# Kernel optimization log

Measured on AMD Instinct MI355X. Metric: run time of the kernel, lower is better.

Reference implementation:

```python
import jax, jax.numpy as jnp
import numpy as np

DIM = 1024
HEADS = 16
HEAD_DIM = DIM // HEADS
B, S = 4, 4096


def setup_inputs() -> dict:
    key = jax.random.key(0)
    ks = jax.random.split(key, 8)
    sc = 1.0 / np.sqrt(DIM)
    return {
        "x": jax.random.normal(ks[0], (B, S, DIM), dtype=jnp.float32),
        "Wq": jax.random.normal(ks[1], (DIM, DIM), dtype=jnp.float32) * sc,
        "Wk": jax.random.normal(ks[2], (DIM, DIM), dtype=jnp.float32) * sc,
        "Wv": jax.random.normal(ks[3], (DIM, DIM), dtype=jnp.float32) * sc,
        "Wp": jax.random.normal(ks[4], (DIM, DIM), dtype=jnp.float32) * sc,
        "bp": jnp.zeros((DIM,), dtype=jnp.float32),
        "conv_w": jax.random.normal(ks[5], (DIM, 3), dtype=jnp.float32) * (1.0 / np.sqrt(3.0)),
        "conv_b": jnp.zeros((DIM,), dtype=jnp.float32),
    }


def reference(x, Wq, Wk, Wv, Wp, bp, conv_w, conv_b):
    b, s, d = x.shape
    # projections -> [b, h, n, hd] (torch Linear: x @ W.T)
    def split_heads(t):
        return t.reshape(b, s, HEADS, HEAD_DIM).transpose(0, 2, 1, 3)
    q = split_heads(x @ Wq.T)
    k = split_heads(x @ Wk.T)
    v = split_heads(x @ Wv.T)
    # ELU(+1) feature map
    q = jax.nn.elu(q) + 1.0
    k = jax.nn.elu(k) + 1.0
    # global kv-state and k-state
    kv_state = jnp.einsum('bhnd,bhne->bhde', k, v)   # [b,h,hd,hd]
    k_state = k.sum(axis=2)                          # [b,h,hd]
    attn_out = jnp.einsum('bhnd,bhde->bhne', q, kv_state)
    denom = jnp.maximum(jnp.einsum('bhnd,bhd->bhn', q, k_state), 1e-6)[..., None]
    attn_out = (attn_out / denom).transpose(0, 2, 1, 3).reshape(b, s, d)
    # depthwise conv1d, kernel=3, padding=1 (per-channel)
    xp = jnp.pad(x, ((0, 0), (1, 1), (0, 0)))        # [b, s+2, d]
    local = (xp[:, :-2, :] * conv_w[:, 0]
             + xp[:, 1:-1, :] * conv_w[:, 1]
             + xp[:, 2:, :] * conv_w[:, 2]) + conv_b
    return (attn_out + local) @ Wp.T + bp
```

## Files before the change

### kernel.cpp

```cpp
#include <hip/hip_runtime.h>
#include <hip/hip_bf16.h>
#include <stdint.h>

#define DIMN 1024
#define HEADS 16
#define HD 64
#define BATCH 4
#define SEQ 4096
#define M_TOT (BATCH*SEQ)

typedef __attribute__((ext_vector_type(8))) __bf16 bf16x8;
typedef __attribute__((ext_vector_type(4))) __bf16 bf16x4;
typedef __attribute__((ext_vector_type(4))) float f32x4;

__device__ __forceinline__ void gload_lds16(const void* g, void* l) {
  __builtin_amdgcn_global_load_lds(
      (const __attribute__((address_space(1))) void*)(uintptr_t)g,
      (__attribute__((address_space(3))) void*)(uint32_t)(uintptr_t)l,
      16, 0, 0);
}

__device__ __forceinline__ uint32_t swz128(uint32_t off) {
  return off ^ (((off >> 7) & 7) << 4);
}

__device__ __forceinline__ void lfence() { asm volatile("" ::: "memory"); }
__device__ __forceinline__ void barx() { lfence(); __builtin_amdgcn_s_barrier(); lfence(); }

__global__ __launch_bounds__(256) void cast_all_kernel(const float* __restrict__ x,
                                                       const float* __restrict__ wq,
                                                       const float* __restrict__ wk,
                                                       const float* __restrict__ wv,
                                                       const float* __restrict__ wp,
                                                       __bf16* __restrict__ xb,
                                                       __bf16* __restrict__ wqb,
                                                       __bf16* __restrict__ wkb,
                                                       __bf16* __restrict__ wvb,
                                                       __bf16* __restrict__ wpb) {
  int i = blockIdx.x * 256 + threadIdx.x;
  const float* src; __bf16* dst; int j;
  if (i < 4194304)      { src = x;  dst = xb;  j = i; }
  else {
    int t = i - 4194304;
    int w = t >> 18; j = t & 262143;
    if      (w == 0) { src = wq; dst = wqb; }
    else if (w == 1) { src = wk; dst = wkb; }
    else if (w == 2) { src = wv; dst = wvb; }
    else             { src = wp; dst = wpb; }
  }
  f32x4 v = ((const f32x4*)src)[j];
  bf16x4 o;
  o[0] = (__bf16)v[0]; o[1] = (__bf16)v[1]; o[2] = (__bf16)v[2]; o[3] = (__bf16)v[3];
  ((bf16x4*)dst)[j] = o;
}

template <int MODE, int NT>
__global__ __launch_bounds__(512, 2) void gemm256(const __bf16* __restrict__ A,
                                                  const __bf16* __restrict__ Bw,
                                                  void* __restrict__ Cout,
                                                  const float* __restrict__ bias) {
  __shared__ char lds[131072];
  const int KB = DIMN * 2;
  const int NKT = DIMN / 64;
  const int bid = blockIdx.x;
  const int x = bid & 7, jj = bid >> 3;
  const int n_t = jj % NT, m_t = (jj / NT) * 8 + x;
  const int m0 = m_t * 256, n0 = n_t * 256;
  const int tid = threadIdx.x;
  const int lane = tid & 63;
  const int wave = tid >> 6;
  const int wm = wave >> 2;
  const int wn = wave & 3;
  const int r16 = lane & 15, r4 = lane >> 4;

  const uint32_t s_off0 = tid * 16;
  const uint32_t s_off1 = 8192 + tid * 16;
  const uint32_t s_row0 = s_off0 >> 7, s_row1 = s_off1 >> 7;
  const uint32_t s_col0 = (s_off0 ^ ((s_row0 & 7) << 4)) & 127;
  const uint32_t s_col1 = (s_off1 ^ ((s_row1 & 7) << 4)) & 127;

  const char* Ab = (const char*)A + (size_t)m0 * KB;
  const char* Bb = (const char*)Bw + (size_t)n0 * KB;

  auto STAGE = [&](int op, int h, int kt, int b) {
    const char* gb = (op ? Bb : Ab) + (size_t)(h * 128) * KB + kt * 128;
    char* lb = lds + op * 65536 + b * 32768 + h * 16384;
    gload_lds16(gb + s_row0 * KB + s_col0, lb + s_off0);
    gload_lds16(gb + s_row1 * KB + s_col1, lb + s_off1);
  };

  uint32_t axk[2];
#pragma unroll
  for (int k = 0; k < 2; ++k) axk[k] = (uint32_t)(k * 64 + r4 * 16) ^ ((r16 & 7) << 4);

  f32x4 acc[8][4] = {};
  bf16x8 bc[4][2];

  STAGE(1, 0, 0, 0); STAGE(1, 1, 0, 0); STAGE(0, 0, 0, 0); STAGE(0, 1, 0, 0);
  STAGE(1, 0, 1, 1); STAGE(1, 1, 1, 1); STAGE(0, 0, 1, 1);
  asm volatile("s_waitcnt vmcnt(6)" ::: "memory");
  barx();

  for (int kt = 0; kt < NKT; ++kt) {
    const int p = kt & 1;
    const char* abuf = lds + p * 32768;
    const char* bbuf = lds + 65536 + p * 32768;

    {
      bf16x8 af[2][2];
#pragma unroll
      for (int nf = 0; nf < 4; ++nf)
#pragma unroll
        for (int k = 0; k < 2; ++k)
          bc[nf][k] = *(const bf16x8*)(bbuf + (nf >> 1) * 16384 +
                        (((nf & 1) * 64 + wn * 16 + r16) << 7) + axk[k]);
#pragma unroll
      for (int i = 0; i < 2; ++i)
#pragma unroll
        for (int k = 0; k < 2; ++k)
          af[i][k] = *(const bf16x8*)(abuf + ((i * 32 + wm * 16 + r16) << 7) + axk[k]);
      if (kt + 1 < NKT) STAGE(0, 1, kt + 1, (kt + 1) & 1);
      barx();
      __builtin_amdgcn_s_setprio(1);
#pragma unroll
      for (int i = 0; i < 2; ++i)
#pragma unroll
        for (int nf = 0; nf < 4; ++nf)
#pragma unroll
          for (int k = 0; k < 2; ++k)
            acc[i][nf] = __builtin_amdgcn_mfma_f32_16x16x32_bf16(bc[nf][k], af[i][k], acc[i][nf], 0, 0, 0);
      __builtin_amdgcn_s_setprio(0);
    }
    {
      bf16x8 af[2][2];
#pragma unroll
      for (int i = 0; i < 2; ++i)
#pragma unroll
        for (int k = 0; k < 2; ++k)
          af[i][k] = *(const bf16x8*)(abuf + (((2 + i) * 32 + wm * 16 + r16) << 7) + axk[k]);
      if (kt + 2 < NKT) STAGE(1, 0, kt + 2, p);
      barx();
      __builtin_amdgcn_s_setprio(1);
#pragma unroll
      for (int i = 0; i < 2; ++i)
#pragma unroll
        for (int nf = 0; nf < 4; ++nf)
#pragma unroll
          for (int k = 0; k < 2; ++k)
            acc[2 + i][nf] = __builtin_amdgcn_mfma_f32_16x16x32_bf16(bc[nf][k], af[i][k], acc[2 + i][nf], 0, 0, 0);
      __builtin_amdgcn_s_setprio(0);
    }
    {
      bf16x8 af[2][2];
#pragma unroll
      for (int i = 0; i < 2; ++i)
#pragma unroll
        for (int k = 0; k < 2; ++k)
          af[i][k] = *(const bf16x8*)(abuf + 16384 + ((i * 32 + wm * 16 + r16) << 7) + axk[k]);
      if (kt + 2 < NKT) STAGE(1, 1, kt + 2, p);
      barx();
      __builtin_amdgcn_s_setprio(1);
#pragma unroll
      for (int i = 0; i < 2; ++i)
#pragma unroll
        for (int nf = 0; nf < 4; ++nf)
#pragma unroll
          for (int k = 0; k < 2; ++k)
            acc[4 + i][nf] = __builtin_amdgcn_mfma_f32_16x16x32_bf16(bc[nf][k], af[i][k], acc[4 + i][nf], 0, 0, 0);
      __builtin_amdgcn_s_setprio(0);
    }
    {
      bf16x8 af[2][2];
#pragma unroll
      for (int i = 0; i < 2; ++i)
#pragma unroll
        for (int k = 0; k < 2; ++k)
          af[i][k] = *(const bf16x8*)(abuf + 16384 + (((2 + i) * 32 + wm * 16 + r16) << 7) + axk[k]);
      if (kt + 2 < NKT) STAGE(0, 0, kt + 2, p);
      if (kt == NKT - 2) { asm volatile("s_waitcnt vmcnt(0)" ::: "memory"); }
      else if (kt < NKT - 2) { asm volatile("s_waitcnt vmcnt(6)" ::: "memory"); }
      barx();
      __builtin_amdgcn_s_setprio(1);
#pragma unroll
      for (int i = 0; i < 2; ++i)
#pragma unroll
        for (int nf = 0; nf < 4; ++nf)
#pragma unroll
          for (int k = 0; k < 2; ++k)
            acc[6 + i][nf] = __builtin_amdgcn_mfma_f32_16x16x32_bf16(bc[nf][k], af[i][k], acc[6 + i][nf], 0, 0, 0);
      __builtin_amdgcn_s_setprio(0);
    }
  }

  const int wsel = n0 >> 10;
  const bool do_elu = (MODE == 3) && (wsel < 2);
#pragma unroll
  for (int mf = 0; mf < 8; ++mf) {
    const int row = m0 + mf * 32 + wm * 16 + r16;
#pragma unroll
    for (int nf = 0; nf < 4; ++nf) {
      const int n = n0 + nf * 64 + wn * 16 + r4 * 4;
      if (MODE == 2) {
        f32x4 bq = *(const f32x4*)(bias + n);
        f32x4 o;
#pragma unroll
        for (int r = 0; r < 4; ++r) o[r] = acc[mf][nf][r] + bq[r];
        *(f32x4*)&((float*)Cout)[(size_t)row * DIMN + n] = o;
      } else {
        bf16x4 o;
#pragma unroll
        for (int r = 0; r < 4; ++r) {
          float v = acc[mf][nf][r];
          if (do_elu) v = (v > 0.f) ? (v + 1.f) : __expf(v);
          o[r] = (__bf16)v;
        }
        int c = n & 1023;
        int h = c >> 6, e2 = c & 63;
        int b = row >> 12, s = row & 4095;
        *(bf16x4*)&((__bf16*)Cout)[(size_t)wsel * 16777216 +
                    ((size_t)((b * HEADS + h) * SEQ + s)) * HD + e2] = o;
      }
    }
  }
}

__global__ __launch_bounds__(256) void kv_state_mfma(const __bf16* __restrict__ kp,
                                                     const __bf16* __restrict__ vb,
                                                     float* __restrict__ kv,
                                                     float* __restrict__ ks) {
  __shared__ __bf16 kt[64][136];
  __shared__ __bf16 vt[80][136];
  const int bid = blockIdx.x;
  const int bh = bid >> 2, nc = bid & 3;
  const int tid = threadIdx.x;
  const int lane = tid & 63;
  const int wave = tid >> 6;
  const int r16 = lane & 15, r4 = lane >> 4;

  for (int i = tid; i < 16 * 136; i += 256) {
    int rr = i / 136;
    vt[64 + rr][i - rr * 136] = (rr == 0) ? (__bf16)1.0f : (__bf16)0.0f;
  }

  const int trow = tid >> 1;
  const int tcol = (tid & 1) * 32;

  f32x4 acc[5] = {};
  bf16x8 kr[4], vr[4];

  size_t gb = ((size_t)bh * SEQ + nc * 1024 + trow) * HD + tcol;
#pragma unroll
  for (int q = 0; q < 4; ++q) {
    kr[q] = *(const bf16x8*)(kp + gb + q * 8);
    vr[q] = *(const bf16x8*)(vb + gb + q * 8);
  }

  for (int t = 0; t < 8; ++t) {
    __syncthreads();
#pragma unroll
    for (int q = 0; q < 4; ++q)
#pragma unroll
      for (int j = 0; j < 8; ++j) {
        kt[tcol + q * 8 + j][trow] = kr[q][j];
        vt[tcol + q * 8 + j][trow] = vr[q][j];
      }
    __syncthreads();
    if (t < 7) {
      size_t gb2 = ((size_t)bh * SEQ + nc * 1024 + (t + 1) * 128 + trow) * HD + tcol;
#pragma unroll
      for (int q = 0; q < 4; ++q) {
        kr[q] = *(const bf16x8*)(kp + gb2 + q * 8);
        vr[q] = *(const bf16x8*)(vb + gb2 + q * 8);
      }
    }
#pragma unroll
    for (int ksl = 0; ksl < 4; ++ksl) {
      bf16x8 af = *(const bf16x8*)&kt[wave * 16 + r16][ksl * 32 + r4 * 8];
#pragma unroll
      for (int eb = 0; eb < 5; ++eb) {
        bf16x8 bf_ = *(const bf16x8*)&vt[eb * 16 + r16][ksl * 32 + r4 * 8];
        acc[eb] = __builtin_amdgcn_mfma_f32_16x16x32_bf16(af, bf_, acc[eb], 0, 0, 0);
      }
    }
  }

#pragma unroll
  for (int eb = 0; eb < 4; ++eb)
#pragma unroll
    for (int r = 0; r < 4; ++r) {
      int d = wave * 16 + r4 * 4 + r;
      atomicAdd(&kv[(size_t)bh * 4096 + d * 64 + eb * 16 + r16], acc[eb][r]);
    }
  if (r16 == 0) {
#pragma unroll
    for (int r = 0; r < 4; ++r)
      atomicAdd(&ks[bh * 64 + wave * 16 + r4 * 4 + r], acc[4][r]);
  }
}

__global__ __launch_bounds__(256) void prep_kv_kernel(const float* __restrict__ kv,
                                                      const float* __restrict__ ks,
                                                      __bf16* __restrict__ kvb) {
  const int bh = blockIdx.x;
  const int tid = threadIdx.x;
  for (int idx = tid; idx < 80 * 64; idx += 256) {
    int e = idx >> 6, d = idx & 63;
    float v;
    if (e < 64)       v = kv[(size_t)bh * 4096 + d * 64 + e];
    else if (e == 64) v = ks[bh * 64 + d];
    else              v = 0.f;
    kvb[(size_t)bh * 5120 + idx] = (__bf16)v;
  }
}

__global__ __launch_bounds__(256) void attn_local_mfma(const __bf16* __restrict__ qp,
                                                       const __bf16* __restrict__ kvb,
                                                       const float* __restrict__ x,
                                                       const float* __restrict__ conv_w,
                                                       const float* __restrict__ conv_b,
                                                       __bf16* __restrict__ y) {
  __shared__ __bf16 qs[128 * 64];
  __shared__ __bf16 bs[80 * 64];
  const int bid = blockIdx.x;
  const int bh = bid >> 5;
  const int chunk = bid & 31;
  const int tid = threadIdx.x;
  const int lane = tid & 63;
  const int wave = tid >> 6;
  const int r16 = lane & 15, r4 = lane >> 4;

  const char* qbase  = (const char*)(qp + ((size_t)bh * SEQ + chunk * 128) * HD);
  const char* kvbase = (const char*)(kvb + (size_t)bh * 5120);
#pragma unroll
  for (int t = 0; t < 4; ++t) {
    int c = t * 4 + wave;
    uint32_t off = c * 1024 + lane * 16;
    gload_lds16(qbase + swz128(off), ((char*)qs) + off);
  }
#pragma unroll
  for (int t = 0; t < 3; ++t) {
    int c = t * 4 + wave;
    if (c < 10) {
      uint32_t off = c * 1024 + lane * 16;
      gload_lds16(kvbase + swz128(off), ((char*)bs) + off);
    }
  }
  __syncthreads();

  f32x4 acc[2][5] = {};
#pragma unroll
  for (int kstep = 0; kstep < 2; ++kstep) {
    bf16x8 af[2], bfr[5];
#pragma unroll
    for (int i = 0; i < 2; ++i) {
      uint32_t off = (wave * 32 + i * 16 + r16) * 128 + kstep * 64 + r4 * 16;
      af[i] = *(const bf16x8*)(((char*)qs) + swz128(off));
    }
#pragma unroll
    for (int j = 0; j < 5; ++j) {
      uint32_t off = (j * 16 + r16) * 128 + kstep * 64 + r4 * 16;
      bfr[j] = *(const bf16x8*)(((char*)bs) + swz128(off));
    }
#pragma unroll
    for (int i = 0; i < 2; ++i)
#pragma unroll
      for (int j = 0; j < 5; ++j)
        acc[i][j] = __builtin_amdgcn_mfma_f32_16x16x32_bf16(af[i], bfr[j], acc[i][j], 0, 0, 0);
  }

  const int b = bh >> 4, h = bh & 15;
  float w0[4], w1[4], w2[4], bb[4];
#pragma unroll
  for (int j = 0; j < 4; ++j) {
    int c = h * HD + j * 16 + r16;
    w0[j] = conv_w[c * 3 + 0]; w1[j] = conv_w[c * 3 + 1]; w2[j] = conv_w[c * 3 + 2];
    bb[j] = conv_b[c];
  }
#pragma unroll
  for (int i = 0; i < 2; ++i) {
#pragma unroll
    for (int r = 0; r < 4; ++r) {
      int s = chunk * 128 + wave * 32 + i * 16 + r4 * 4 + r;
      size_t m = (size_t)b * SEQ + s;
      float den = fmaxf(__shfl(acc[i][4][r], lane & 48), 1e-6f);
      float inv = 1.0f / den;
#pragma unroll
      for (int j = 0; j < 4; ++j) {
        int c = h * HD + j * 16 + r16;
        float xm = x[m * DIMN + c];
        float xl = (s > 0)       ? x[(m - 1) * DIMN + c] : 0.f;
        float xr = (s < SEQ - 1) ? x[(m + 1) * DIMN + c] : 0.f;
        float val = acc[i][j][r] * inv
                  + xl * w0[j] + xm * w1[j] + xr * w2[j] + bb[j];
        y[m * DIMN + c] = (__bf16)val;
      }
    }
  }
}

extern "C" void kernel_launch(void* const* d_in, const int* in_sizes, int n_in,
                              void* d_out, int out_size, void* d_ws, size_t ws_size,
                              hipStream_t stream) {
  const float* x  = (const float*)d_in[0];
  const float* Wq = (const float*)d_in[1];
  const float* Wk = (const float*)d_in[2];
  const float* Wv = (const float*)d_in[3];
  const float* Wp = (const float*)d_in[4];
  const float* bp = (const float*)d_in[5];
  const float* cw = (const float*)d_in[6];
  const float* cb = (const float*)d_in[7];
  float* out = (float*)d_out;

  char* ws = (char*)d_ws;
  const size_t MB = 1024 * 1024;
  __bf16* xb  = (__bf16*)(ws);
  __bf16* y   = xb;
  __bf16* qp  = (__bf16*)(ws + 32 * MB);
  __bf16* kp  = (__bf16*)(ws + 64 * MB);
  __bf16* vb  = (__bf16*)(ws + 96 * MB);
  __bf16* wqb = (__bf16*)(ws + 128 * MB);
  __bf16* wkb = (__bf16*)(ws + 130 * MB);
  __bf16* wvb = (__bf16*)(ws + 132 * MB);
  __bf16* wpb = (__bf16*)(ws + 134 * MB);
  float*  kv  = (float*)(ws + 136 * MB);
  float*  ks  = (float*)(ws + 137 * MB);
  __bf16* kvb = wqb;

  cast_all_kernel<<<20480, 256, 0, stream>>>(x, Wq, Wk, Wv, Wp, xb, wqb, wkb, wvb, wpb);

  gemm256<3, 12><<<768, 512, 0, stream>>>(xb, wqb, qp, nullptr);

  hipMemsetAsync(kv, 0, 64 * 4096 * 4 + 64 * 64 * 4, stream);
  kv_state_mfma<<<256, 256, 0, stream>>>(kp, vb, kv, ks);
  prep_kv_kernel<<<64, 256, 0, stream>>>(kv, ks, kvb);

  attn_local_mfma<<<2048, 256, 0, stream>>>(qp, kvb, x, cw, cb, y);

  gemm256<2, 4><<<256, 512, 0, stream>>>(y, wpb, out, bp);
}
```

Baseline: 237.1 us.

## Load GEMM B operand directly from global into registers, halving LDS

The weight (B) tile is no longer staged through LDS. Each wave now loads its B fragments straight from global memory into double-buffered registers one k-step ahead, and the A pipeline is restructured into two phases per k-tile. This halves LDS usage from 128KB to 64KB, which may raise occupancy and removes the B LDS traffic. In exchange, each of the 4 wm waves fetches the same B data redundantly, register pressure grows, and the vmcnt accounting becomes more fragile.

```diff
diff --git a/kernel.cpp b/kernel.cpp
--- a/kernel.cpp
+++ b/kernel.cpp
@@ -59,7 +59,7 @@
                                                   const __bf16* __restrict__ Bw,
                                                   void* __restrict__ Cout,
                                                   const float* __restrict__ bias) {
-  __shared__ char lds[131072];
+  __shared__ char lds[65536];
   const int KB = DIMN * 2;
   const int NKT = DIMN / 64;
   const int bid = blockIdx.x;
@@ -80,116 +80,86 @@
   const uint32_t s_col1 = (s_off1 ^ ((s_row1 & 7) << 4)) & 127;
 
   const char* Ab = (const char*)A + (size_t)m0 * KB;
-  const char* Bb = (const char*)Bw + (size_t)n0 * KB;
-
-  auto STAGE = [&](int op, int h, int kt, int b) {
-    const char* gb = (op ? Bb : Ab) + (size_t)(h * 128) * KB + kt * 128;
-    char* lb = lds + op * 65536 + b * 32768 + h * 16384;
+  const char* Brow = (const char*)Bw + (size_t)(n0 + wn * 16 + r16) * KB + r4 * 16;
+
+  auto STAGE = [&](int h, int kt, int b) {
+    const char* gb = Ab + (size_t)(h * 128) * KB + kt * 128;
+    char* lb = lds + b * 32768 + h * 16384;
     gload_lds16(gb + s_row0 * KB + s_col0, lb + s_off0);
     gload_lds16(gb + s_row1 * KB + s_col1, lb + s_off1);
   };
 
+  auto loadB = [&](bf16x8 (&dst)[4][2], int kt) {
+#pragma unroll
+    for (int nf = 0; nf < 4; ++nf)
+#pragma unroll
+      for (int k = 0; k < 2; ++k)
+        dst[nf][k] = *(const bf16x8*)(Brow + (size_t)nf * 64 * KB + kt * 128 + k * 64);
+  };
+
   uint32_t axk[2];
 #pragma unroll
   for (int k = 0; k < 2; ++k) axk[k] = (uint32_t)(k * 64 + r4 * 16) ^ ((r16 & 7) << 4);
 
   f32x4 acc[8][4] = {};
-  bf16x8 bc[4][2];
-
-  STAGE(1, 0, 0, 0); STAGE(1, 1, 0, 0); STAGE(0, 0, 0, 0); STAGE(0, 1, 0, 0);
-  STAGE(1, 0, 1, 1); STAGE(1, 1, 1, 1); STAGE(0, 0, 1, 1);
-  asm volatile("s_waitcnt vmcnt(6)" ::: "memory");
+  bf16x8 bcE[4][2], bcO[4][2];
+
+  auto phaseA = [&](int kt, int buf, bf16x8 (&bcur)[4][2], bf16x8 (&bnxt)[4][2]) {
+    bf16x8 af[4][2];
+#pragma unroll
+    for (int mf = 0; mf < 4; ++mf)
+#pragma unroll
+      for (int k = 0; k < 2; ++k)
+        af[mf][k] = *(const bf16x8*)(lds + buf * 32768 +
+                      ((mf * 32 + wm * 16 + r16) << 7) + axk[k]);
+    if (kt + 1 < NKT) { loadB(bnxt, kt + 1); STAGE(1, kt + 1, buf ^ 1); }
+    if (kt == NKT - 1) { asm volatile("s_waitcnt vmcnt(0)" ::: "memory"); }
+    else               { asm volatile("s_waitcnt vmcnt(12)" ::: "memory"); }
+    barx();
+    __builtin_amdgcn_s_setprio(1);
+#pragma unroll
+    for (int mf = 0; mf < 4; ++mf)
+#pragma unroll
+      for (int nf = 0; nf < 4; ++nf)
+#pragma unroll
+        for (int k = 0; k < 2; ++k)
+          acc[mf][nf] = __builtin_amdgcn_mfma_f32_16x16x32_bf16(bcur[nf][k], af[mf][k], acc[mf][nf], 0, 0, 0);
+    __builtin_amdgcn_s_setprio(0);
+  };
+
+  auto phaseB = [&](int kt, int buf, bf16x8 (&bcur)[4][2]) {
+    bf16x8 af[4][2];
+#pragma unroll
+    for (int mf = 0; mf < 4; ++mf)
+#pragma unroll
+      for (int k = 0; k < 2; ++k)
+        af[mf][k] = *(const bf16x8*)(lds + buf * 32768 + 16384 +
+                      ((mf * 32 + wm * 16 + r16) << 7) + axk[k]);
+    if (kt + 2 < NKT) STAGE(0, kt + 2, buf);
+    if (kt == NKT - 2)      { asm volatile("s_waitcnt vmcnt(10)" ::: "memory"); }
+    else if (kt < NKT - 2)  { asm volatile("s_waitcnt vmcnt(12)" ::: "memory"); }
+    barx();
+    __builtin_amdgcn_s_setprio(1);
+#pragma unroll
+    for (int mf = 0; mf < 4; ++mf)
+#pragma unroll
+      for (int nf = 0; nf < 4; ++nf)
+#pragma unroll
+        for (int k = 0; k < 2; ++k)
+          acc[4 + mf][nf] = __builtin_amdgcn_mfma_f32_16x16x32_bf16(bcur[nf][k], af[mf][k], acc[4 + mf][nf], 0, 0, 0);
+    __builtin_amdgcn_s_setprio(0);
+  };
+
+  loadB(bcE, 0);
+  STAGE(0, 0, 0); STAGE(1, 0, 0); STAGE(0, 1, 1);
+  asm volatile("s_waitcnt vmcnt(4)" ::: "memory");
   barx();
 
-  for (int kt = 0; kt < NKT; ++kt) {
-    const int p = kt & 1;
-    const char* abuf = lds + p * 32768;
-    const char* bbuf = lds + 65536 + p * 32768;
-
-    {
-      bf16x8 af[2][2];
-#pragma unroll
-      for (int nf = 0; nf < 4; ++nf)
-#pragma unroll
-        for (int k = 0; k < 2; ++k)
-          bc[nf][k] = *(const bf16x8*)(bbuf + (nf >> 1) * 16384 +
-                        (((nf & 1) * 64 + wn * 16 + r16) << 7) + axk[k]);
-#pragma unroll
-      for (int i = 0; i < 2; ++i)
-#pragma unroll
-        for (int k = 0; k < 2; ++k)
-          af[i][k] = *(const bf16x8*)(abuf + ((i * 32 + wm * 16 + r16) << 7) + axk[k]);
-      if (kt + 1 < NKT) STAGE(0, 1, kt + 1, (kt + 1) & 1);
-      barx();
-      __builtin_amdgcn_s_setprio(1);
-#pragma unroll
-      for (int i = 0; i < 2; ++i)
-#pragma unroll
-        for (int nf = 0; nf < 4; ++nf)
-#pragma unroll
-          for (int k = 0; k < 2; ++k)
-            acc[i][nf] = __builtin_amdgcn_mfma_f32_16x16x32_bf16(bc[nf][k], af[i][k], acc[i][nf], 0, 0, 0);
-      __builtin_amdgcn_s_setprio(0);
-    }
-    {
-      bf16x8 af[2][2];
-#pragma unroll
-      for (int i = 0; i < 2; ++i)
-#pragma unroll
-        for (int k = 0; k < 2; ++k)
-          af[i][k] = *(const bf16x8*)(abuf + (((2 + i) * 32 + wm * 16 + r16) << 7) + axk[k]);
-      if (kt + 2 < NKT) STAGE(1, 0, kt + 2, p);
-      barx();
-      __builtin_amdgcn_s_setprio(1);
-#pragma unroll
-      for (int i = 0; i < 2; ++i)
-#pragma unroll
-        for (int nf = 0; nf < 4; ++nf)
-#pragma unroll
-          for (int k = 0; k < 2; ++k)
-            acc[2 + i][nf] = __builtin_amdgcn_mfma_f32_16x16x32_bf16(bc[nf][k], af[i][k], acc[2 + i][nf], 0, 0, 0);
-      __builtin_amdgcn_s_setprio(0);
-    }
-    {
-      bf16x8 af[2][2];
-#pragma unroll
-      for (int i = 0; i < 2; ++i)
-#pragma unroll
-        for (int k = 0; k < 2; ++k)
-          af[i][k] = *(const bf16x8*)(abuf + 16384 + ((i * 32 + wm * 16 + r16) << 7) + axk[k]);
-      if (kt + 2 < NKT) STAGE(1, 1, kt + 2, p);
-      barx();
-      __builtin_amdgcn_s_setprio(1);
-#pragma unroll
-      for (int i = 0; i < 2; ++i)
-#pragma unroll
-        for (int nf = 0; nf < 4; ++nf)
-#pragma unroll
-          for (int k = 0; k < 2; ++k)
-            acc[4 + i][nf] = __builtin_amdgcn_mfma_f32_16x16x32_bf16(bc[nf][k], af[i][k], acc[4 + i][nf], 0, 0, 0);
-      __builtin_amdgcn_s_setprio(0);
-    }
-    {
-      bf16x8 af[2][2];
-#pragma unroll
-      for (int i = 0; i < 2; ++i)
-#pragma unroll
-        for (int k = 0; k < 2; ++k)
-          af[i][k] = *(const bf16x8*)(abuf + 16384 + (((2 + i) * 32 + wm * 16 + r16) << 7) + axk[k]);
-      if (kt + 2 < NKT) STAGE(0, 0, kt + 2, p);
-      if (kt == NKT - 2) { asm volatile("s_waitcnt vmcnt(0)" ::: "memory"); }
-      else if (kt < NKT - 2) { asm volatile("s_waitcnt vmcnt(6)" ::: "memory"); }
-      barx();
-      __builtin_amdgcn_s_setprio(1);
-#pragma unroll
-      for (int i = 0; i < 2; ++i)
-#pragma unroll
-        for (int nf = 0; nf < 4; ++nf)
-#pragma unroll
-          for (int k = 0; k < 2; ++k)
-            acc[6 + i][nf] = __builtin_amdgcn_mfma_f32_16x16x32_bf16(bc[nf][k], af[i][k], acc[6 + i][nf], 0, 0, 0);
-      __builtin_amdgcn_s_setprio(0);
-    }
+  for (int kt = 0; kt < NKT; kt += 2) {
+    phaseA(kt, 0, bcE, bcO);
+    phaseB(kt, 0, bcE);
+    phaseA(kt + 1, 1, bcO, bcE);
+    phaseB(kt + 1, 1, bcO);
   }
 
   const int wsel = n0 >> 10;
```

New measurement: 283.9 us. 19.7% more time.

## Stage QKV epilogue through LDS for coalesced stores and fuse kv prep into attention

Applied to the files above, without the earlier changes.

The QKV projection epilogue now writes bf16 results into LDS with a swizzle, then reads back full 32-byte row segments so each thread issues wide contiguous head-major global stores instead of scattered 8-byte stores. The separate prep_kv kernel is removed: the attention kernel converts the fp32 kv/ks state to bf16 directly into shared memory. The memset is also moved ahead of the cast kernel. The cost is extra barriers per mf iteration in the epilogue and redundant per-block conversion of the kv state across 32 chunks.

```diff
diff --git a/kernel.cpp b/kernel.cpp
--- a/kernel.cpp
+++ b/kernel.cpp
@@ -194,19 +194,27 @@
 
   const int wsel = n0 >> 10;
   const bool do_elu = (MODE == 3) && (wsel < 2);
-#pragma unroll
-  for (int mf = 0; mf < 8; ++mf) {
-    const int row = m0 + mf * 32 + wm * 16 + r16;
-#pragma unroll
-    for (int nf = 0; nf < 4; ++nf) {
-      const int n = n0 + nf * 64 + wn * 16 + r4 * 4;
-      if (MODE == 2) {
+  if (MODE == 2) {
+#pragma unroll
+    for (int mf = 0; mf < 8; ++mf) {
+      const int row = m0 + mf * 32 + wm * 16 + r16;
+#pragma unroll
+      for (int nf = 0; nf < 4; ++nf) {
+        const int n = n0 + nf * 64 + wn * 16 + r4 * 4;
         f32x4 bq = *(const f32x4*)(bias + n);
         f32x4 o;
 #pragma unroll
         for (int r = 0; r < 4; ++r) o[r] = acc[mf][nf][r] + bq[r];
         *(f32x4*)&((float*)Cout)[(size_t)row * DIMN + n] = o;
-      } else {
+      }
+    }
+  } else {
+#pragma unroll 1
+    for (int mf = 0; mf < 8; ++mf) {
+      barx();
+      const int wrow = wm * 16 + r16;
+#pragma unroll
+      for (int nf = 0; nf < 4; ++nf) {
         bf16x4 o;
 #pragma unroll
         for (int r = 0; r < 4; ++r) {
@@ -214,12 +222,24 @@
           if (do_elu) v = (v > 0.f) ? (v + 1.f) : __expf(v);
           o[r] = (__bf16)v;
         }
-        int c = n & 1023;
-        int h = c >> 6, e2 = c & 63;
-        int b = row >> 12, s = row & 4095;
-        *(bf16x4*)&((__bf16*)Cout)[(size_t)wsel * 16777216 +
-                    ((size_t)((b * HEADS + h) * SEQ + s)) * HD + e2] = o;
-      }
+        uint32_t off = (uint32_t)(wrow * 512 + (nf * 64 + wn * 16 + r4 * 4) * 2);
+        *(bf16x4*)(lds + (off ^ ((wrow & 7) << 4))) = o;
+      }
+      barx();
+      const int lrow = tid >> 4;
+      const uint32_t colb = (tid & 15) * 32;
+      uint32_t ro = (uint32_t)(lrow * 512 + colb) ^ ((lrow & 7) << 4);
+      bf16x8 v0 = *(const bf16x8*)(lds + ro);
+      bf16x8 v1 = *(const bf16x8*)(lds + (ro ^ 16));
+      const int row = m0 + mf * 32 + lrow;
+      const int col = n0 + (int)(colb >> 1);
+      const int c = col & 1023;
+      const int h = c >> 6, e2 = c & 63;
+      const int b = row >> 12, s = row & 4095;
+      __bf16* dst = (__bf16*)Cout + (size_t)wsel * 16777216 +
+                    ((size_t)((b * HEADS + h) * SEQ + s)) * HD + e2;
+      *(bf16x8*)dst = v0;
+      *(bf16x8*)(dst + 8) = v1;
     }
   }
 }
@@ -298,23 +318,9 @@
   }
 }
 
-__global__ __launch_bounds__(256) void prep_kv_kernel(const float* __restrict__ kv,
-                                                      const float* __restrict__ ks,
-                                                      __bf16* __restrict__ kvb) {
-  const int bh = blockIdx.x;
-  const int tid = threadIdx.x;
-  for (int idx = tid; idx < 80 * 64; idx += 256) {
-    int e = idx >> 6, d = idx & 63;
-    float v;
-    if (e < 64)       v = kv[(size_t)bh * 4096 + d * 64 + e];
-    else if (e == 64) v = ks[bh * 64 + d];
-    else              v = 0.f;
-    kvb[(size_t)bh * 5120 + idx] = (__bf16)v;
-  }
-}
-
 __global__ __launch_bounds__(256) void attn_local_mfma(const __bf16* __restrict__ qp,
-                                                       const __bf16* __restrict__ kvb,
+                                                       const float* __restrict__ kv,
+                                                       const float* __restrict__ ks,
                                                        const float* __restrict__ x,
                                                        const float* __restrict__ conv_w,
                                                        const float* __restrict__ conv_b,
@@ -329,21 +335,19 @@
   const int wave = tid >> 6;
   const int r16 = lane & 15, r4 = lane >> 4;
 
-  const char* qbase  = (const char*)(qp + ((size_t)bh * SEQ + chunk * 128) * HD);
-  const char* kvbase = (const char*)(kvb + (size_t)bh * 5120);
+  const char* qbase = (const char*)(qp + ((size_t)bh * SEQ + chunk * 128) * HD);
 #pragma unroll
   for (int t = 0; t < 4; ++t) {
     int c = t * 4 + wave;
     uint32_t off = c * 1024 + lane * 16;
     gload_lds16(qbase + swz128(off), ((char*)qs) + off);
   }
-#pragma unroll
-  for (int t = 0; t < 3; ++t) {
-    int c = t * 4 + wave;
-    if (c < 10) {
-      uint32_t off = c * 1024 + lane * 16;
-      gload_lds16(kvbase + swz128(off), ((char*)bs) + off);
-    }
+  for (int i = tid; i < 80 * 64; i += 256) {
+    int e = i >> 6, d = i & 63;
+    float v = (e < 64) ? kv[(size_t)bh * 4096 + d * 64 + e]
+                       : (e == 64 ? ks[bh * 64 + d] : 0.f);
+    uint32_t off = (uint32_t)(i * 2);
+    *(__bf16*)(((char*)bs) + swz128(off)) = (__bf16)v;
   }
   __syncthreads();
 
@@ -424,17 +428,16 @@
   __bf16* wpb = (__bf16*)(ws + 134 * MB);
   float*  kv  = (float*)(ws + 136 * MB);
   float*  ks  = (float*)(ws + 137 * MB);
-  __bf16* kvb = wqb;
+
+  hipMemsetAsync(kv, 0, 64 * 4096 * 4 + 64 * 64 * 4, stream);
 
   cast_all_kernel<<<20480, 256, 0, stream>>>(x, Wq, Wk, Wv, Wp, xb, wqb, wkb, wvb, wpb);
 
   gemm256<3, 12><<<768, 512, 0, stream>>>(xb, wqb, qp, nullptr);
 
-  hipMemsetAsync(kv, 0, 64 * 4096 * 4 + 64 * 64 * 4, stream);
   kv_state_mfma<<<256, 256, 0, stream>>>(kp, vb, kv, ks);
-  prep_kv_kernel<<<64, 256, 0, stream>>>(kv, ks, kvb);
-
-  attn_local_mfma<<<2048, 256, 0, stream>>>(qp, kvb, x, cw, cb, y);
+
+  attn_local_mfma<<<2048, 256, 0, stream>>>(qp, kv, ks, x, cw, cb, y);
 
   gemm256<2, 4><<<256, 512, 0, stream>>>(y, wpb, out, bp);
 }
```

New measurement: 397.6 us. 67.7% more time.
